# Optimization experiments

Measured on AMD Instinct MI355X. Metric: run time of the kernel, lower is better.

Reference implementation:

```python
import jax, jax.numpy as jnp
import numpy as np

B, T, D, A = 4, 4096, 1024, 64
RINGS = 2

def _build_graph_matrix(A, rings):
    # W[a_dst, a_src] = 1/len(neigh) for src in {a_dst-rings..a_dst+rings} within bounds (mean reduce)
    W = np.zeros((A, A), dtype=np.float32)
    for a in range(A):
        neigh = [n for n in range(a - rings, a + rings + 1) if 0 <= n < A]
        W[a, neigh] = 1.0 / len(neigh)
    return jnp.asarray(W)

def setup_inputs() -> dict:
    key = jax.random.key(0)
    k0, k1, k2 = jax.random.split(key, 3)
    x = jax.random.normal(k0, (B, T, D), dtype=jnp.float32)
    # contiguous-ish 1D region assignment of tokens to anchors
    assign = jnp.sort(jax.random.randint(k1, (T,), 0, A)).astype(jnp.int32)
    counts = jnp.clip(jnp.zeros((A,), jnp.float32).at[assign].add(1.0), 1.0, None)
    W_proj = jax.random.normal(k2, (D, D), dtype=jnp.float32) * (1.0 / np.sqrt(D))
    gate = jnp.float32(0.1)
    W_graph = _build_graph_matrix(A, RINGS)
    return {"x": x, "W_proj": W_proj, "gate": gate, "assign": assign,
            "W_graph": W_graph, "counts": counts, "hops": 1}

def reference(x, W_proj, gate, assign, W_graph, counts, hops):
    Bx, Tx, Dx = x.shape
    Ax = counts.shape[0]
    # pool_per_anchor (mean): scatter-add tokens into anchors, divide by counts
    anchor = jnp.zeros((Bx, Ax, Dx), x.dtype).at[:, assign, :].add(x)
    anchor = anchor / counts[None, :, None]
    # neighbor_aggregate: out = einsum('bcd,ac->bad', out, W) per hop
    agg = anchor
    for _ in range(max(1, int(hops))):
        agg = jnp.einsum('ac,bcd->bad', W_graph, agg)
    # broadcast_from_anchor: gather each token's anchor feature
    fb = agg[:, assign, :]  # [B,T,D]
    # residual with gated linear projection (dropout identity in eval)
    return x + (fb @ W_proj.T) * jnp.tanh(gate)
```

## Files before the change

kernel.cpp:

```cpp
#include <hip/hip_runtime.h>
#include <cmath>


typedef __attribute__((ext_vector_type(8))) short bf16x8;
typedef __attribute__((ext_vector_type(4))) float f32x4;

__device__ inline short f2bf(float f) {
    unsigned u = __float_as_uint(f);
    unsigned r = (u + 0x7FFFu + ((u >> 16) & 1u)) >> 16;
    return (short)r;
}

__global__ void prep_kernel(const int* __restrict__ assign, int T, int A,
                            int* __restrict__ seg,
                            const float* __restrict__ Wg, const int* __restrict__ hops,
                            float* __restrict__ M,
                            const float* __restrict__ Wp, short* __restrict__ Wpb,
                            long long n8) {
    __shared__ float cur[64 * 64];
    __shared__ float nxt[64 * 64];
    if (blockIdx.x == 0) {
        int a = threadIdx.x;
        if (a <= A) {
            int lo = 0, hi = T;
            while (lo < hi) { int mid = (lo + hi) >> 1; if (assign[mid] < a) lo = mid + 1; else hi = mid; }
            seg[a] = lo;
        }
    } else if (blockIdx.x == 1) {
        int n = A * A;
        for (int i = threadIdx.x; i < n; i += blockDim.x) cur[i] = Wg[i];
        int h = hops[0]; if (h < 1) h = 1;
        for (int it = 1; it < h; ++it) {
            __syncthreads();
            for (int i = threadIdx.x; i < n; i += blockDim.x) {
                int r = i / A, c = i % A;
                float s = 0.f;
                for (int k = 0; k < A; ++k) s += Wg[r * A + k] * cur[k * A + c];
                nxt[i] = s;
            }
            __syncthreads();
            for (int i = threadIdx.x; i < n; i += blockDim.x) cur[i] = nxt[i];
        }
        __syncthreads();
        for (int i = threadIdx.x; i < n; i += blockDim.x) M[i] = cur[i];
    } else {
        long long i = (long long)(blockIdx.x - 2) * blockDim.x + threadIdx.x;
        if (i < n8) {
            const float4* p = (const float4*)Wp + i * 2;
            float4 v0 = p[0], v1 = p[1];
            short4* q = (short4*)Wpb + i * 2;
            short4 o0, o1;
            o0.x = f2bf(v0.x); o0.y = f2bf(v0.y); o0.z = f2bf(v0.z); o0.w = f2bf(v0.w);
            o1.x = f2bf(v1.x); o1.y = f2bf(v1.y); o1.z = f2bf(v1.z); o1.w = f2bf(v1.w);
            q[0] = o0; q[1] = o1;
        }
    }
}

__global__ void anchor_kernel(const float* __restrict__ x, const float* __restrict__ counts,
                              const int* __restrict__ seg, float* __restrict__ anchor,
                              int T, int D, int A) {
    int b = blockIdx.x / A, a = blockIdx.x % A;
    int t0 = seg[a], t1 = seg[a + 1];
    float inv = 1.0f / counts[a];
    int rs = D >> 2;
    const float4* x4 = (const float4*)x + (size_t)b * T * rs;
    float4* an4 = (float4*)anchor + (size_t)blockIdx.x * rs;
    for (int d4 = threadIdx.x; d4 < rs; d4 += blockDim.x) {
        float4 acc = make_float4(0.f, 0.f, 0.f, 0.f);
        const float4* p = x4 + (size_t)t0 * rs + d4;
        int t = t0;
        for (; t + 8 <= t1; t += 8) {
            float4 v0 = p[0];
            float4 v1 = p[(size_t)rs];
            float4 v2 = p[(size_t)2 * rs];
            float4 v3 = p[(size_t)3 * rs];
            float4 v4 = p[(size_t)4 * rs];
            float4 v5 = p[(size_t)5 * rs];
            float4 v6 = p[(size_t)6 * rs];
            float4 v7 = p[(size_t)7 * rs];
            acc.x += ((v0.x + v1.x) + (v2.x + v3.x)) + ((v4.x + v5.x) + (v6.x + v7.x));
            acc.y += ((v0.y + v1.y) + (v2.y + v3.y)) + ((v4.y + v5.y) + (v6.y + v7.y));
            acc.z += ((v0.z + v1.z) + (v2.z + v3.z)) + ((v4.z + v5.z) + (v6.z + v7.z));
            acc.w += ((v0.w + v1.w) + (v2.w + v3.w)) + ((v4.w + v5.w) + (v6.w + v7.w));
            p += (size_t)8 * rs;
        }
        for (; t < t1; ++t) {
            float4 v = *p;
            acc.x += v.x; acc.y += v.y; acc.z += v.z; acc.w += v.w;
            p += rs;
        }
        an4[d4] = make_float4(acc.x * inv, acc.y * inv, acc.z * inv, acc.w * inv);
    }
}

__global__ void agg_kernel(const float* __restrict__ anchor, const float* __restrict__ M,
                           short* __restrict__ aggb, int D, int A) {
    int b = blockIdx.x / A, a = blockIdx.x % A;
    __shared__ float row[64];
    if (threadIdx.x < A) row[threadIdx.x] = M[a * A + threadIdx.x];
    __syncthreads();
    int rs = D >> 2;
    const float4* an4 = (const float4*)anchor;
    short4* ag4 = (short4*)aggb;
    for (int d4 = threadIdx.x; d4 < rs; d4 += blockDim.x) {
        float4 acc = make_float4(0.f, 0.f, 0.f, 0.f);
        for (int c = 0; c < A; ++c) {
            float w = row[c];
            float4 v = an4[((size_t)b * A + c) * rs + d4];
            acc.x += w * v.x; acc.y += w * v.y; acc.z += w * v.z; acc.w += w * v.w;
        }
        short4 o;
        o.x = f2bf(acc.x); o.y = f2bf(acc.y); o.z = f2bf(acc.z); o.w = f2bf(acc.w);
        ag4[(size_t)blockIdx.x * rs + d4] = o;
    }
}

__global__ __launch_bounds__(256) void ymfma_kernel(
        const short* __restrict__ Agb, const short* __restrict__ Wpb,
        float* __restrict__ Y, int D) {
    int wave = threadIdx.x >> 6;
    int lane = threadIdx.x & 63;
    int rBase = blockIdx.x * 16;
    int dBase = blockIdx.y * 64 + wave * 16;
    int rc = lane & 15;
    int kOff = (lane >> 4) * 8;
    const short* aPtr = Agb + (size_t)(rBase + rc) * D + kOff;
    const short* bPtr = Wpb + (size_t)(dBase + rc) * D + kOff;
    f32x4 acc = {0.f, 0.f, 0.f, 0.f};
    #pragma unroll 8
    for (int k = 0; k < D; k += 32) {
        bf16x8 af = *(const bf16x8*)(aPtr + k);
        bf16x8 bf = *(const bf16x8*)(bPtr + k);
        acc = __builtin_amdgcn_mfma_f32_16x16x32_bf16(af, bf, acc, 0, 0, 0);
    }
    int orow = (lane >> 4) * 4;
    #pragma unroll
    for (int j = 0; j < 4; ++j)
        Y[(size_t)(rBase + orow + j) * D + dBase + rc] = acc[j];
}

#define OROWS 8
__global__ void out_kernel(const float* __restrict__ x, const float* __restrict__ Y,
                           const int* __restrict__ assign, const float* __restrict__ gate,
                           float* __restrict__ out, int T, int D, int A) {
    float tg = tanhf(gate[0]);
    int rs = D >> 2;
    int bt0 = blockIdx.x * OROWS;
    const float4* x4 = (const float4*)x;
    const float4* y4 = (const float4*)Y;
    float4* o4 = (float4*)out;
    #pragma unroll
    for (int r = 0; r < OROWS; ++r) {
        int bt = bt0 + r;
        int b = bt / T;
        int t = bt - b * T;
        int a = assign[t];
        const float4* yr = y4 + ((size_t)b * A + a) * rs;
        for (int d4 = threadIdx.x; d4 < rs; d4 += blockDim.x) {
            float4 xv = x4[(size_t)bt * rs + d4];
            float4 yv = yr[d4];
            o4[(size_t)bt * rs + d4] = make_float4(xv.x + tg * yv.x, xv.y + tg * yv.y,
                                                   xv.z + tg * yv.z, xv.w + tg * yv.w);
        }
    }
}

extern "C" void kernel_launch(void* const* d_in, const int* in_sizes, int n_in,
                              void* d_out, int out_size, void* d_ws, size_t ws_size,
                              hipStream_t stream) {
    const float* x      = (const float*)d_in[0];
    const float* Wp     = (const float*)d_in[1];
    const float* gate   = (const float*)d_in[2];
    const int*   assign = (const int*)d_in[3];
    const float* Wg     = (const float*)d_in[4];
    const float* counts = (const float*)d_in[5];
    const int*   hops   = (const int*)d_in[6];
    float* out = (float*)d_out;

    int T = in_sizes[3];
    int A = in_sizes[5];
    int D = (int)(sqrt((double)in_sizes[1]) + 0.5);
    int B = (int)(in_sizes[0] / ((long long)T * D));
    int R = B * A;

    float* anchor = (float*)d_ws;
    float* Y      = anchor + (size_t)R * D;
    float* M      = Y + (size_t)R * D;
    short* Agb    = (short*)(M + (size_t)A * A);
    short* Wpb    = Agb + (size_t)R * D;
    int*   seg    = (int*)(Wpb + (size_t)D * D);

    long long n8 = (long long)D * D / 8;
    int prepBlocks = 2 + (int)((n8 + 255) / 256);
    prep_kernel<<<prepBlocks, 256, 0, stream>>>(assign, T, A, seg, Wg, hops, M, Wp, Wpb, n8);
    anchor_kernel<<<R, 256, 0, stream>>>(x, counts, seg, anchor, T, D, A);
    agg_kernel<<<R, 256, 0, stream>>>(anchor, M, Agb, D, A);
    dim3 g(R / 16, D / 64);
    ymfma_kernel<<<g, 256, 0, stream>>>(Agb, Wpb, Y, D);
    out_kernel<<<B * T / OROWS, 256, 0, stream>>>(x, Y, assign, gate, out, T, D, A);
}
```

Baseline: 64.39 us.

## Fuse prep into anchor pooling and reorder graph mix after projection GEMM

Merges the segment search, graph-matrix power and weight bf16 conversion into the anchor pooling kernel, so one launch and the seg buffer round trip disappear. Anchors are now written directly as bf16. By linearity, the projection GEMM is applied to the pooled anchors first and the graph mixing runs on the fp32 projected result afterwards. This removes a dependent launch, though the mixing now reads fp32 Z instead of fp32 anchors, and bf16 rounding moves before the mean aggregation.

After: 60.09 us. 1.07x faster.

```diff
diff --git a/kernel.cpp b/kernel.cpp
--- a/kernel.cpp
+++ b/kernel.cpp
@@ -5,47 +5,69 @@
 typedef __attribute__((ext_vector_type(8))) short bf16x8;
 typedef __attribute__((ext_vector_type(4))) float f32x4;
 
+#define OROWS 8
+
 __device__ inline short f2bf(float f) {
     unsigned u = __float_as_uint(f);
-    unsigned r = (u + 0x7FFFu + ((u >> 16) & 1u)) >> 16;
-    return (short)r;
-}
-
-__global__ void prep_kernel(const int* __restrict__ assign, int T, int A,
-                            int* __restrict__ seg,
-                            const float* __restrict__ Wg, const int* __restrict__ hops,
-                            float* __restrict__ M,
-                            const float* __restrict__ Wp, short* __restrict__ Wpb,
-                            long long n8) {
-    __shared__ float cur[64 * 64];
-    __shared__ float nxt[64 * 64];
-    if (blockIdx.x == 0) {
-        int a = threadIdx.x;
-        if (a <= A) {
-            int lo = 0, hi = T;
-            while (lo < hi) { int mid = (lo + hi) >> 1; if (assign[mid] < a) lo = mid + 1; else hi = mid; }
-            seg[a] = lo;
-        }
-    } else if (blockIdx.x == 1) {
-        int n = A * A;
-        for (int i = threadIdx.x; i < n; i += blockDim.x) cur[i] = Wg[i];
-        int h = hops[0]; if (h < 1) h = 1;
-        for (int it = 1; it < h; ++it) {
-            __syncthreads();
-            for (int i = threadIdx.x; i < n; i += blockDim.x) {
-                int r = i / A, c = i % A;
-                float s = 0.f;
-                for (int k = 0; k < A; ++k) s += Wg[r * A + k] * cur[k * A + c];
-                nxt[i] = s;
+    return (short)((u + 0x7FFFu + ((u >> 16) & 1u)) >> 16);
+}
+__device__ inline int lbound(const int* __restrict__ a, int n, int v) {
+    int lo = 0, hi = n;
+    while (lo < hi) { int m = (lo + hi) >> 1; if (a[m] < v) lo = m + 1; else hi = m; }
+    return lo;
+}
+
+__global__ __launch_bounds__(256) void prepanchor_kernel(
+        const float* __restrict__ x, const float* __restrict__ counts,
+        const int* __restrict__ assign, const float* __restrict__ Wg,
+        const int* __restrict__ hops, const float* __restrict__ Wp,
+        short* __restrict__ anchorb, short* __restrict__ Wpb, float* __restrict__ M,
+        int T, int D, int A, int R) {
+    __shared__ float s0[4096];
+    __shared__ float s1[4096];
+    int bid = blockIdx.x, tid = threadIdx.x;
+    int rs = D >> 2;
+    if (bid < R) {
+        int b = bid / A, a = bid - (bid / A) * A;
+        int* sT = (int*)s1;
+        if (tid < 2) sT[tid] = lbound(assign, T, a + tid);
+        __syncthreads();
+        int t0 = sT[0], t1 = sT[1];
+        float inv = 1.0f / counts[a];
+        const float4* x4 = (const float4*)x + (size_t)b * T * rs;
+        short4* an4 = (short4*)anchorb + (size_t)bid * rs;
+        for (int d4 = tid; d4 < rs; d4 += 256) {
+            float4 acc = make_float4(0.f, 0.f, 0.f, 0.f);
+            const float4* p = x4 + (size_t)t0 * rs + d4;
+            int t = t0;
+            for (; t + 8 <= t1; t += 8) {
+                float4 v0 = p[0];
+                float4 v1 = p[(size_t)rs];
+                float4 v2 = p[(size_t)2 * rs];
+                float4 v3 = p[(size_t)3 * rs];
+                float4 v4 = p[(size_t)4 * rs];
+                float4 v5 = p[(size_t)5 * rs];
+                float4 v6 = p[(size_t)6 * rs];
+                float4 v7 = p[(size_t)7 * rs];
+                acc.x += ((v0.x + v1.x) + (v2.x + v3.x)) + ((v4.x + v5.x) + (v6.x + v7.x));
+                acc.y += ((v0.y + v1.y) + (v2.y + v3.y)) + ((v4.y + v5.y) + (v6.y + v7.y));
+                acc.z += ((v0.z + v1.z) + (v2.z + v3.z)) + ((v4.z + v5.z) + (v6.z + v7.z));
+                acc.w += ((v0.w + v1.w) + (v2.w + v3.w)) + ((v4.w + v5.w) + (v6.w + v7.w));
+                p += (size_t)8 * rs;
             }
-            __syncthreads();
-            for (int i = threadIdx.x; i < n; i += blockDim.x) cur[i] = nxt[i];
-        }
-        __syncthreads();
-        for (int i = threadIdx.x; i < n; i += blockDim.x) M[i] = cur[i];
-    } else {
-        long long i = (long long)(blockIdx.x - 2) * blockDim.x + threadIdx.x;
-        if (i < n8) {
+            for (; t < t1; ++t) {
+                float4 v = *p;
+                acc.x += v.x; acc.y += v.y; acc.z += v.z; acc.w += v.w;
+                p += rs;
+            }
+            short4 o;
+            o.x = f2bf(acc.x * inv); o.y = f2bf(acc.y * inv);
+            o.z = f2bf(acc.z * inv); o.w = f2bf(acc.w * inv);
+            an4[d4] = o;
+        }
+    } else if (bid < R + 256) {
+        long long n8 = (long long)D * D / 8;
+        for (long long i = (long long)(bid - R) * 256 + tid; i < n8; i += 256LL * 256LL) {
             const float4* p = (const float4*)Wp + i * 2;
             float4 v0 = p[0], v1 = p[1];
             short4* q = (short4*)Wpb + i * 2;
@@ -54,71 +76,29 @@
             o1.x = f2bf(v1.x); o1.y = f2bf(v1.y); o1.z = f2bf(v1.z); o1.w = f2bf(v1.w);
             q[0] = o0; q[1] = o1;
         }
-    }
-}
-
-__global__ void anchor_kernel(const float* __restrict__ x, const float* __restrict__ counts,
-                              const int* __restrict__ seg, float* __restrict__ anchor,
-                              int T, int D, int A) {
-    int b = blockIdx.x / A, a = blockIdx.x % A;
-    int t0 = seg[a], t1 = seg[a + 1];
-    float inv = 1.0f / counts[a];
-    int rs = D >> 2;
-    const float4* x4 = (const float4*)x + (size_t)b * T * rs;
-    float4* an4 = (float4*)anchor + (size_t)blockIdx.x * rs;
-    for (int d4 = threadIdx.x; d4 < rs; d4 += blockDim.x) {
-        float4 acc = make_float4(0.f, 0.f, 0.f, 0.f);
-        const float4* p = x4 + (size_t)t0 * rs + d4;
-        int t = t0;
-        for (; t + 8 <= t1; t += 8) {
-            float4 v0 = p[0];
-            float4 v1 = p[(size_t)rs];
-            float4 v2 = p[(size_t)2 * rs];
-            float4 v3 = p[(size_t)3 * rs];
-            float4 v4 = p[(size_t)4 * rs];
-            float4 v5 = p[(size_t)5 * rs];
-            float4 v6 = p[(size_t)6 * rs];
-            float4 v7 = p[(size_t)7 * rs];
-            acc.x += ((v0.x + v1.x) + (v2.x + v3.x)) + ((v4.x + v5.x) + (v6.x + v7.x));
-            acc.y += ((v0.y + v1.y) + (v2.y + v3.y)) + ((v4.y + v5.y) + (v6.y + v7.y));
-            acc.z += ((v0.z + v1.z) + (v2.z + v3.z)) + ((v4.z + v5.z) + (v6.z + v7.z));
-            acc.w += ((v0.w + v1.w) + (v2.w + v3.w)) + ((v4.w + v5.w) + (v6.w + v7.w));
-            p += (size_t)8 * rs;
-        }
-        for (; t < t1; ++t) {
-            float4 v = *p;
-            acc.x += v.x; acc.y += v.y; acc.z += v.z; acc.w += v.w;
-            p += rs;
-        }
-        an4[d4] = make_float4(acc.x * inv, acc.y * inv, acc.z * inv, acc.w * inv);
-    }
-}
-
-__global__ void agg_kernel(const float* __restrict__ anchor, const float* __restrict__ M,
-                           short* __restrict__ aggb, int D, int A) {
-    int b = blockIdx.x / A, a = blockIdx.x % A;
-    __shared__ float row[64];
-    if (threadIdx.x < A) row[threadIdx.x] = M[a * A + threadIdx.x];
-    __syncthreads();
-    int rs = D >> 2;
-    const float4* an4 = (const float4*)anchor;
-    short4* ag4 = (short4*)aggb;
-    for (int d4 = threadIdx.x; d4 < rs; d4 += blockDim.x) {
-        float4 acc = make_float4(0.f, 0.f, 0.f, 0.f);
-        for (int c = 0; c < A; ++c) {
-            float w = row[c];
-            float4 v = an4[((size_t)b * A + c) * rs + d4];
-            acc.x += w * v.x; acc.y += w * v.y; acc.z += w * v.z; acc.w += w * v.w;
-        }
-        short4 o;
-        o.x = f2bf(acc.x); o.y = f2bf(acc.y); o.z = f2bf(acc.z); o.w = f2bf(acc.w);
-        ag4[(size_t)blockIdx.x * rs + d4] = o;
-    }
-}
-
-__global__ __launch_bounds__(256) void ymfma_kernel(
+    } else {
+        int n = A * A;
+        for (int i = tid; i < n; i += 256) s0[i] = Wg[i];
+        int h = hops[0]; if (h < 1) h = 1;
+        for (int it = 1; it < h; ++it) {
+            __syncthreads();
+            for (int i = tid; i < n; i += 256) {
+                int r = i / A, c = i - (i / A) * A;
+                float s = 0.f;
+                for (int k = 0; k < A; ++k) s += Wg[r * A + k] * s0[k * A + c];
+                s1[i] = s;
+            }
+            __syncthreads();
+            for (int i = tid; i < n; i += 256) s0[i] = s1[i];
+        }
+        __syncthreads();
+        for (int i = tid; i < n; i += 256) M[i] = s0[i];
+    }
+}
+
+__global__ __launch_bounds__(256) void zgemm_kernel(
         const short* __restrict__ Agb, const short* __restrict__ Wpb,
-        float* __restrict__ Y, int D) {
+        float* __restrict__ Z, int D) {
     int wave = threadIdx.x >> 6;
     int lane = threadIdx.x & 63;
     int rBase = blockIdx.x * 16;
@@ -137,13 +117,34 @@
     int orow = (lane >> 4) * 4;
     #pragma unroll
     for (int j = 0; j < 4; ++j)
-        Y[(size_t)(rBase + orow + j) * D + dBase + rc] = acc[j];
-}
-
-#define OROWS 8
-__global__ void out_kernel(const float* __restrict__ x, const float* __restrict__ Y,
-                           const int* __restrict__ assign, const float* __restrict__ gate,
-                           float* __restrict__ out, int T, int D, int A) {
+        Z[(size_t)(rBase + orow + j) * D + dBase + rc] = acc[j];
+}
+
+__global__ __launch_bounds__(256) void mix_kernel(
+        const float* __restrict__ Z, const float* __restrict__ M,
+        float* __restrict__ Y, int D, int A) {
+    int b = blockIdx.x / A, a = blockIdx.x - (blockIdx.x / A) * A;
+    __shared__ float row[64];
+    if (threadIdx.x < A) row[threadIdx.x] = M[a * A + threadIdx.x];
+    __syncthreads();
+    int rs = D >> 2;
+    const float4* z4 = (const float4*)Z + (size_t)b * A * rs;
+    float4* y4 = (float4*)Y + (size_t)blockIdx.x * rs;
+    for (int d4 = threadIdx.x; d4 < rs; d4 += 256) {
+        float4 acc = make_float4(0.f, 0.f, 0.f, 0.f);
+        for (int c = 0; c < A; ++c) {
+            float w = row[c];
+            float4 v = z4[(size_t)c * rs + d4];
+            acc.x += w * v.x; acc.y += w * v.y; acc.z += w * v.z; acc.w += w * v.w;
+        }
+        y4[d4] = acc;
+    }
+}
+
+__global__ __launch_bounds__(256) void out_kernel(
+        const float* __restrict__ x, const float* __restrict__ Y,
+        const int* __restrict__ assign, const float* __restrict__ gate,
+        float* __restrict__ out, int T, int D, int A) {
     float tg = tanhf(gate[0]);
     int rs = D >> 2;
     int bt0 = blockIdx.x * OROWS;
@@ -157,7 +158,7 @@
         int t = bt - b * T;
         int a = assign[t];
         const float4* yr = y4 + ((size_t)b * A + a) * rs;
-        for (int d4 = threadIdx.x; d4 < rs; d4 += blockDim.x) {
+        for (int d4 = threadIdx.x; d4 < rs; d4 += 256) {
             float4 xv = x4[(size_t)bt * rs + d4];
             float4 yv = yr[d4];
             o4[(size_t)bt * rs + d4] = make_float4(xv.x + tg * yv.x, xv.y + tg * yv.y,
@@ -184,19 +185,16 @@
     int B = (int)(in_sizes[0] / ((long long)T * D));
     int R = B * A;
 
-    float* anchor = (float*)d_ws;
-    float* Y      = anchor + (size_t)R * D;
-    float* M      = Y + (size_t)R * D;
-    short* Agb    = (short*)(M + (size_t)A * A);
-    short* Wpb    = Agb + (size_t)R * D;
-    int*   seg    = (int*)(Wpb + (size_t)D * D);
-
-    long long n8 = (long long)D * D / 8;
-    int prepBlocks = 2 + (int)((n8 + 255) / 256);
-    prep_kernel<<<prepBlocks, 256, 0, stream>>>(assign, T, A, seg, Wg, hops, M, Wp, Wpb, n8);
-    anchor_kernel<<<R, 256, 0, stream>>>(x, counts, seg, anchor, T, D, A);
-    agg_kernel<<<R, 256, 0, stream>>>(anchor, M, Agb, D, A);
+    float* Z       = (float*)d_ws;
+    float* Y       = Z + (size_t)R * D;
+    float* M       = Y + (size_t)R * D;
+    short* anchorb = (short*)(M + (size_t)A * A);
+    short* Wpb     = anchorb + (size_t)R * D;
+
+    prepanchor_kernel<<<R + 257, 256, 0, stream>>>(x, counts, assign, Wg, hops, Wp,
+                                                   anchorb, Wpb, M, T, D, A, R);
     dim3 g(R / 16, D / 64);
-    ymfma_kernel<<<g, 256, 0, stream>>>(Agb, Wpb, Y, D);
+    zgemm_kernel<<<g, 256, 0, stream>>>(anchorb, Wpb, Z, D);
+    mix_kernel<<<R, 256, 0, stream>>>(Z, M, Y, D, A);
     out_kernel<<<B * T / OROWS, 256, 0, stream>>>(x, Y, assign, gate, out, T, D, A);
 }
```
